# Kernel optimization log

Hardware: AMD Instinct MI355X
Metric: run time of the kernel (lower is better)

Reference implementation:

```python
import jax, jax.numpy as jnp
import numpy as np


def setup_inputs() -> dict:
    key = jax.random.key(0)
    ks = jax.random.split(key, 9)
    B, T, S, E, H = 4, 4096, 4096, 512, 64
    return {
        "x": jax.random.normal(ks[0], (B, T, 1), dtype=jnp.float32),
        "tok_emb": jax.random.normal(ks[1], (B, S, E), dtype=jnp.float32),
        "key_w": jax.random.normal(ks[2], (H, E), dtype=jnp.float32) * 0.05,
        "key_b": jax.random.normal(ks[3], (H,), dtype=jnp.float32) * 0.05,
        "query_w": jax.random.normal(ks[4], (H, 1), dtype=jnp.float32) * 0.05,
        "query_b": jax.random.normal(ks[5], (H,), dtype=jnp.float32) * 0.05,
        "value_w": jax.random.normal(ks[6], (H, E), dtype=jnp.float32) * 0.05,
        "proj_w": jax.random.normal(ks[7], (1, H), dtype=jnp.float32) * 0.05,
        "proj_b": jax.random.normal(ks[8], (1,), dtype=jnp.float32) * 0.05,
    }


def reference(x, tok_emb, key_w, key_b, query_w, query_b, value_w, proj_w, proj_b):
    # k = tanh(Linear(tok_emb))            [B,S,H]
    k = jnp.tanh(jnp.einsum("bse,he->bsh", tok_emb, key_w) + key_b)
    # q = tanh(Linear(x)); x last dim is 1 [B,T,H]
    q = jnp.tanh(jnp.einsum("btu,hu->bth", x, query_w) + query_b)
    scale = k.shape[-1] ** (-0.5)
    wei = jnp.einsum("bth,bsh->bts", q, k) * scale  # [B,T,S]
    # NOTE: softmax over dim=-2 (the query/T axis), faithful to the original
    wei = jax.nn.softmax(wei, axis=-2)
    v = jnp.tanh(jnp.einsum("bse,he->bsh", tok_emb, value_w))  # [B,S,H]
    out = jnp.tanh(jnp.einsum("bts,bsh->bth", wei, v))         # [B,T,H]
    out = jnp.einsum("bth,oh->bto", out, proj_w) + proj_b      # [B,T,1]
    return jnp.squeeze(out, axis=-1)                            # [B,T]
```

## Files before the change

kernel.cpp:

```cpp
#include <hip/hip_runtime.h>
#include <math.h>

#define BB 4
#define TT 4096
#define SS 4096
#define EE 512
#define HH 64
#define NN 128
#define XR 6.0f


typedef __attribute__((ext_vector_type(8))) __bf16 bf16x8;
typedef __attribute__((ext_vector_type(16))) float f32x16;

__device__ __forceinline__ unsigned short f2b(float f) {
  unsigned int u = __float_as_uint(f);
  return (unsigned short)((u + 0x7FFFu + ((u >> 16) & 1u)) >> 16);
}

__device__ __forceinline__ float fast_tanh(float v) {
  float e = __expf(fminf(60.0f, 2.0f * v));
  return (e - 1.0f) * __builtin_amdgcn_rcpf(e + 1.0f);
}

__global__ __launch_bounds__(256) void prep_sm_kernel(
    const float* __restrict__ kw, const float* __restrict__ vw,
    const float* __restrict__ qw, const float* __restrict__ qb,
    const float* __restrict__ x, unsigned int* __restrict__ Wfrag,
    float* __restrict__ Cmat, unsigned short* __restrict__ qnA,
    float* __restrict__ Sm_part, float* __restrict__ Oz) {
  const int blk = blockIdx.x;
  if (blk < 64) {
    int idx = blk * 256 + threadIdx.x;
    int jq = idx & 1;
    int l = (idx >> 1) & 63;
    int ks = (idx >> 7) & 31;
    int nb = idx >> 12;
    int n = nb * 32 + (l & 31);
    int k = ks * 16 + (l >> 5) * 8 + jq * 4;
    const float* row = (n < HH) ? (kw + n * EE + k) : (vw + (n - HH) * EE + k);
    float4 wv = *(const float4*)row;
    Wfrag[idx * 2] = (unsigned int)f2b(wv.x) | ((unsigned int)f2b(wv.y) << 16);
    Wfrag[idx * 2 + 1] =
        (unsigned int)f2b(wv.z) | ((unsigned int)f2b(wv.w) << 16);
  } else if (blk < 128) {
    int idx = (blk - 64) * 256 + threadIdx.x;
    int m = idx >> 7;
    int j = idx & (NN - 1);
    int k = (m * (2 * j + 1)) & 511;
    if (k >= 256) k -= 512;
    Cmat[idx] = cosf((float)k * (float)(M_PI / 256.0));
    if (idx < 8192) ((float4*)Oz)[idx] = make_float4(0.f, 0.f, 0.f, 0.f);
    if (idx < 8192) {
      int h = idx & 63;
      int j2 = idx >> 6;
      float th = (float)M_PI * ((float)j2 + 0.5f) * (1.0f / NN);
      float xj = XR * cosf(th);
      float val = tanhf(fmaf(xj, qw[h], qb[h]));
      int pos =
          (((j2 >> 5) * 4 + (h >> 4)) * 64 + (j2 & 31) + 32 * ((h >> 3) & 1)) *
              8 +
          (h & 7);
      qnA[pos] = f2b(val);
    }
  } else {
    __shared__ float Tm[128][NN + 1];
    int blk2 = blk - 128;
    int b = blk2 >> 5;
    int chunk = blk2 & 31;
    int tid = threadIdx.x;
    if (tid < 128) {
      float xh = x[b * TT + chunk * 128 + tid] * (1.0f / XR);
      xh = fminf(1.0f, fmaxf(-1.0f, xh));
      Tm[tid][0] = 1.0f;
      Tm[tid][1] = xh;
      float x2 = 2.0f * xh;
      float tm2 = 1.0f, tm1 = xh;
#pragma unroll 6
      for (int m = 2; m < NN; ++m) {
        float t = fmaf(x2, tm1, -tm2);
        Tm[tid][m] = t;
        tm2 = tm1;
        tm1 = t;
      }
    }
    __syncthreads();
    if (tid < 128) {
      float s = 0.f;
#pragma unroll 8
      for (int i = 0; i < 128; ++i) s += Tm[i][tid];
      Sm_part[(b * 32 + chunk) * NN + tid] = s;
    }
  }
}

__global__ __launch_bounds__(512) void kvattn_kernel(
    const float* __restrict__ emb, const float* __restrict__ kb,
    const unsigned int* __restrict__ Wfrag, const unsigned short* __restrict__ qnA,
    const float* __restrict__ Cmat, const float* __restrict__ Sm_part,
    float* __restrict__ O) {
  __shared__ __align__(16) char smem[69120];
  unsigned short* A_lds = (unsigned short*)smem;
  unsigned short* ktB = (unsigned short*)smem;
  unsigned short* vB = (unsigned short*)(smem + 8192);
  unsigned short* eA = (unsigned short*)(smem + 16384);
  float* zred = (float*)(smem + 65536);
  float* wql = (float*)(smem + 67840);
  float* izl = (float*)(smem + 68352);
  float* sml = (float*)(smem + 68608);

  const int tid = threadIdx.x;
  const int row0 = blockIdx.x * 64;
  const int bb = row0 >> 12;

  {
    int m = tid >> 3;
    int c8 = tid & 7;
    const float* src = emb + (size_t)(row0 + m) * EE;
    unsigned short* dst = A_lds + (m >> 5) * 16384;
    int ml = m & 31;
    float4 buf[16];
#pragma unroll
    for (int it = 0; it < 16; ++it)
      buf[it] = *(const float4*)(src + (c8 + it * 8) * 4);
#pragma unroll
    for (int it = 0; it < 16; ++it) {
      int k = (c8 + it * 8) * 4;
      float4 v = buf[it];
      int kstep = k >> 4;
      int lane_f = ml + 32 * ((k >> 3) & 1);
      int j = k & 7;
      unsigned int lo = (unsigned int)f2b(v.x) | ((unsigned int)f2b(v.y) << 16);
      unsigned int hi = (unsigned int)f2b(v.z) | ((unsigned int)f2b(v.w) << 16);
      *(uint2*)&dst[(kstep * 64 + lane_f) * 8 + j] = make_uint2(lo, hi);
    }
  }
  if (tid < 128) {
    float s = 0.f;
#pragma unroll 8
    for (int c = 0; c < 32; ++c) s += Sm_part[(bb * 32 + c) * NN + tid];
    sml[tid] = s * ((tid == 0) ? (1.0f / NN) : (2.0f / NN));
  }
  __syncthreads();
  if (tid < 128) {
    float a0 = 0.f, a1 = 0.f, a2 = 0.f, a3 = 0.f;
#pragma unroll
    for (int m = 0; m < NN; m += 4) {
      a0 = fmaf(sml[m], Cmat[m * NN + tid], a0);
      a1 = fmaf(sml[m + 1], Cmat[(m + 1) * NN + tid], a1);
      a2 = fmaf(sml[m + 2], Cmat[(m + 2) * NN + tid], a2);
      a3 = fmaf(sml[m + 3], Cmat[(m + 3) * NN + tid], a3);
    }
    wql[tid] = (a0 + a1) + (a2 + a3);
  }

  const int w8 = tid >> 6;
  const int lane = tid & 63;
  const int w = w8 & 3;
  const int mh = w8 >> 2;
  f32x16 acc = {};
  const bf16x8* Bf = (const bf16x8*)Wfrag;
  const unsigned short* Ah = A_lds + mh * 16384;
#pragma unroll 4
  for (int kstep = 0; kstep < 32; ++kstep) {
    bf16x8 bfr = Bf[(w * 32 + kstep) * 64 + lane];
    bf16x8 a = *(const bf16x8*)&Ah[(kstep * 64 + lane) * 8];
    acc = __builtin_amdgcn_mfma_f32_32x32x16_bf16(a, bfr, acc, 0, 0, 0);
  }
  __syncthreads();

  {
    const int n = w * 32 + (lane & 31);
    if (w < 2) {
      float kbv = kb[n];
      const int ks_h = n >> 4;
      const int off_h = 32 * ((n >> 3) & 1);
      const int jj_h = n & 7;
#pragma unroll
      for (int reg = 0; reg < 16; ++reg) {
        int sl = (reg & 3) + 8 * (reg >> 2) + 4 * (lane >> 5);
        ktB[((mh * 4 + ks_h) * 64 + sl + off_h) * 8 + jj_h] =
            f2b(fast_tanh(acc[reg] + kbv));
      }
    } else {
      int h = n - 64;
      const int nb_h = h >> 5;
      const int lm = h & 31;
#pragma unroll
      for (int reg = 0; reg < 16; ++reg) {
        int sl = (reg & 3) + 8 * (reg >> 2) + 4 * (lane >> 5);
        int s = mh * 32 + sl;
        vB[((nb_h * 4 + (s >> 4)) * 64 + lm + 32 * ((s >> 3) & 1)) * 8 +
           (s & 7)] = f2b(fast_tanh(acc[reg]));
      }
    }
  }
  __syncthreads();

  f32x16 l0 = {};
#pragma unroll
  for (int ks = 0; ks < 4; ++ks) {
    bf16x8 a = *(const bf16x8*)(qnA + ((w * 4 + ks) * 64 + lane) * 8);
    bf16x8 b0 = *(const bf16x8*)&ktB[((mh * 4 + ks) * 64 + lane) * 8];
    l0 = __builtin_amdgcn_mfma_f32_32x32x16_bf16(a, b0, l0, 0, 0, 0);
  }
  float e0[16];
  float zp = 0.f;
#pragma unroll
  for (int r = 0; r < 4; ++r) {
    float4 wq4 = *(const float4*)&wql[w * 32 + 8 * r + 4 * (lane >> 5)];
    float wa[4] = {wq4.x, wq4.y, wq4.z, wq4.w};
#pragma unroll
    for (int c = 0; c < 4; ++c) {
      int reg = 4 * r + c;
      e0[reg] = __expf(l0[reg] * 0.125f);
      zp = fmaf(wa[c], e0[reg], zp);
    }
  }
  zred[(mh * 32 + (lane & 31)) * 9 + w * 2 + (lane >> 5)] = zp;
  __syncthreads();
  if (tid < 64) {
    float sum = 0.f;
#pragma unroll
    for (int k = 0; k < 8; ++k) sum += zred[tid * 9 + k];
    izl[tid] = 1.0f / sum;
  }
  __syncthreads();

  {
    const int s = mh * 32 + (lane & 31);
    const float iz = izl[s];
    const int q0 = w * 4 + (s >> 4);
    const int lof = 32 * ((s >> 3) & 1);
    const int idx = s & 7;
#pragma unroll
    for (int reg = 0; reg < 16; ++reg) {
      int jl = (reg & 3) + 8 * (reg >> 2) + 4 * (lane >> 5);
      eA[(q0 * 64 + jl + lof) * 8 + idx] = f2b(e0[reg] * iz);
    }
  }
  __syncthreads();
  f32x16 o0 = {};
#pragma unroll
  for (int ks = 0; ks < 4; ++ks) {
    bf16x8 a = *(const bf16x8*)&eA[((w * 4 + ks) * 64 + lane) * 8];
    bf16x8 b0 = *(const bf16x8*)&vB[((mh * 4 + ks) * 64 + lane) * 8];
    o0 = __builtin_amdgcn_mfma_f32_32x32x16_bf16(a, b0, o0, 0, 0, 0);
  }
  float* op = O + (size_t)bb * (NN * HH);
  const int h0 = mh * 32 + (lane & 31);
  const int rot = blockIdx.x & 15;
#pragma unroll
  for (int rr = 0; rr < 16; ++rr) {
    int reg = (rr + rot) & 15;
    int j = w * 32 + (reg & 3) + 8 * (reg >> 2) + 4 * (lane >> 5);
    atomicAdd(&op[j * HH + h0], o0[reg]);
  }
}

__global__ __launch_bounds__(256) void final_kernel(
    const float* __restrict__ x, const float* __restrict__ O,
    const float* __restrict__ pw, const float* __restrict__ pb,
    const float* __restrict__ Cmat, float* __restrict__ y) {
  const int idx = blockIdx.x * 256 + threadIdx.x;
  const int b = idx >> 12;
  __shared__ float yl[NN];
  __shared__ float c[NN];
  {
    const int j = threadIdx.x >> 1;
    const int half = threadIdx.x & 1;
    const float4* Ov =
        (const float4*)(O + ((size_t)(b * NN + j) * HH + half * 32));
    const float4* pwv = (const float4*)(pw + half * 32);
    float s = 0.f;
#pragma unroll
    for (int q = 0; q < 8; ++q) {
      float4 ov = Ov[q];
      float4 pv = pwv[q];
      s += fast_tanh(ov.x) * pv.x + fast_tanh(ov.y) * pv.y +
           fast_tanh(ov.z) * pv.z + fast_tanh(ov.w) * pv.w;
    }
    s += __shfl_xor(s, 1, 64);
    if (half == 0) yl[j] = s + pb[0];
  }
  __syncthreads();
  if (threadIdx.x < NN) {
    int m = threadIdx.x;
    double a0 = 0.0, a1 = 0.0;
#pragma unroll 4
    for (int j = 0; j < NN; j += 2) {
      a0 += (double)yl[j] * (double)Cmat[m * NN + j];
      a1 += (double)yl[j + 1] * (double)Cmat[m * NN + j + 1];
    }
    c[m] = (float)((a0 + a1) * ((m == 0 ? 1.0 : 2.0) / NN));
  }
  __syncthreads();
  float xv = x[idx] * (1.0f / XR);
  xv = fminf(1.0f, fmaxf(-1.0f, xv));
  float uu = fmaf(2.0f * xv, xv, -1.0f);
  float tu = 2.0f * uu;
  float be1 = 0.f, be2 = 0.f, bo1 = 0.f, bo2 = 0.f;
  for (int m = 63; m >= 0; --m) {
    float ce = c[2 * m], co = c[2 * m + 1];
    float be = fmaf(tu, be1, ce - be2);
    float bo = fmaf(tu, bo1, co - bo2);
    be2 = be1; be1 = be;
    bo2 = bo1; bo1 = bo;
  }
  float fe = be1 - uu * be2;
  float fo = bo1 - bo2;
  y[idx] = fmaf(xv, fo, fe);
}

extern "C" void kernel_launch(void* const* d_in, const int* in_sizes, int n_in,
                              void* d_out, int out_size, void* d_ws,
                              size_t ws_size, hipStream_t stream) {
  const float* x = (const float*)d_in[0];
  const float* emb = (const float*)d_in[1];
  const float* kw = (const float*)d_in[2];
  const float* kb = (const float*)d_in[3];
  const float* qw = (const float*)d_in[4];
  const float* qb = (const float*)d_in[5];
  const float* vw = (const float*)d_in[6];
  const float* pw = (const float*)d_in[7];
  const float* pb = (const float*)d_in[8];

  float* ws = (float*)d_ws;
  float* O = ws;
  float* Cmat = ws + 32768;
  unsigned short* qnA = (unsigned short*)(Cmat + 16384);
  unsigned int* Wfrag = (unsigned int*)(Cmat + 16384 + 4096);
  float* Sm_part = (float*)(Wfrag + 32768);
  float* y = (float*)d_out;

  prep_sm_kernel<<<256, 256, 0, stream>>>(kw, vw, qw, qb, x, Wfrag, Cmat, qnA,
                                          Sm_part, O);
  kvattn_kernel<<<BB * SS / 64, 512, 0, stream>>>(emb, kb, Wfrag, qnA, Cmat,
                                                  Sm_part, O);
  final_kernel<<<BB * TT / 256, 256, 0, stream>>>(x, O, pw, pb, Cmat, y);
}
```

Baseline: 113.9 us.

## Spread atomic accumulation over eight O slots and reduce in final kernel

Atomic adds into the per-batch output accumulator are spread across eight replicated slots chosen by block index, which reduces contention on the same addresses. The final kernel sums the eight slots before tanh and projection. The embedding load is split into two halves of eight float4 loads, and the kernel gets a launch-bounds occupancy hint of two blocks, both to lower register pressure. In exchange the workspace grows, the prep kernel zeroes the larger O region, and the final kernel does extra reads.

New measurement: 120.6 us. +5.9%, slower.

```diff
diff --git a/kernel.cpp b/kernel.cpp
--- a/kernel.cpp
+++ b/kernel.cpp
@@ -50,7 +50,7 @@
     int k = (m * (2 * j + 1)) & 511;
     if (k >= 256) k -= 512;
     Cmat[idx] = cosf((float)k * (float)(M_PI / 256.0));
-    if (idx < 8192) ((float4*)Oz)[idx] = make_float4(0.f, 0.f, 0.f, 0.f);
+    ((float4*)Oz)[idx] = make_float4(0.f, 0.f, 0.f, 0.f);
     if (idx < 8192) {
       int h = idx & 63;
       int j2 = idx >> 6;
@@ -94,7 +94,7 @@
   }
 }
 
-__global__ __launch_bounds__(512) void kvattn_kernel(
+__global__ __launch_bounds__(512, 2) void kvattn_kernel(
     const float* __restrict__ emb, const float* __restrict__ kb,
     const unsigned int* __restrict__ Wfrag, const unsigned short* __restrict__ qnA,
     const float* __restrict__ Cmat, const float* __restrict__ Sm_part,
@@ -119,20 +119,25 @@
     const float* src = emb + (size_t)(row0 + m) * EE;
     unsigned short* dst = A_lds + (m >> 5) * 16384;
     int ml = m & 31;
-    float4 buf[16];
-#pragma unroll
-    for (int it = 0; it < 16; ++it)
-      buf[it] = *(const float4*)(src + (c8 + it * 8) * 4);
-#pragma unroll
-    for (int it = 0; it < 16; ++it) {
-      int k = (c8 + it * 8) * 4;
-      float4 v = buf[it];
-      int kstep = k >> 4;
-      int lane_f = ml + 32 * ((k >> 3) & 1);
-      int j = k & 7;
-      unsigned int lo = (unsigned int)f2b(v.x) | ((unsigned int)f2b(v.y) << 16);
-      unsigned int hi = (unsigned int)f2b(v.z) | ((unsigned int)f2b(v.w) << 16);
-      *(uint2*)&dst[(kstep * 64 + lane_f) * 8 + j] = make_uint2(lo, hi);
+#pragma unroll
+    for (int half = 0; half < 2; ++half) {
+      float4 buf[8];
+#pragma unroll
+      for (int it = 0; it < 8; ++it)
+        buf[it] = *(const float4*)(src + (c8 + (half * 8 + it) * 8) * 4);
+#pragma unroll
+      for (int it = 0; it < 8; ++it) {
+        int k = (c8 + (half * 8 + it) * 8) * 4;
+        float4 v = buf[it];
+        int kstep = k >> 4;
+        int lane_f = ml + 32 * ((k >> 3) & 1);
+        int j = k & 7;
+        unsigned int lo =
+            (unsigned int)f2b(v.x) | ((unsigned int)f2b(v.y) << 16);
+        unsigned int hi =
+            (unsigned int)f2b(v.z) | ((unsigned int)f2b(v.w) << 16);
+        *(uint2*)&dst[(kstep * 64 + lane_f) * 8 + j] = make_uint2(lo, hi);
+      }
     }
   }
   if (tid < 128) {
@@ -247,7 +252,7 @@
     bf16x8 b0 = *(const bf16x8*)&vB[((mh * 4 + ks) * 64 + lane) * 8];
     o0 = __builtin_amdgcn_mfma_f32_32x32x16_bf16(a, b0, o0, 0, 0, 0);
   }
-  float* op = O + (size_t)bb * (NN * HH);
+  float* op = O + ((size_t)bb * 8 + (blockIdx.x & 7)) * (NN * HH);
   const int h0 = mh * 32 + (lane & 31);
   const int rot = blockIdx.x & 15;
 #pragma unroll
@@ -269,16 +274,27 @@
   {
     const int j = threadIdx.x >> 1;
     const int half = threadIdx.x & 1;
-    const float4* Ov =
-        (const float4*)(O + ((size_t)(b * NN + j) * HH + half * 32));
     const float4* pwv = (const float4*)(pw + half * 32);
+    float4 ov[8];
+#pragma unroll
+    for (int q = 0; q < 8; ++q) ov[q] = make_float4(0.f, 0.f, 0.f, 0.f);
+#pragma unroll
+    for (int slot = 0; slot < 8; ++slot) {
+      const float4* Os =
+          (const float4*)(O + (((size_t)(b * 8 + slot) * NN + j) * HH) +
+                          half * 32);
+#pragma unroll
+      for (int q = 0; q < 8; ++q) {
+        float4 t = Os[q];
+        ov[q].x += t.x; ov[q].y += t.y; ov[q].z += t.z; ov[q].w += t.w;
+      }
+    }
     float s = 0.f;
 #pragma unroll
     for (int q = 0; q < 8; ++q) {
-      float4 ov = Ov[q];
       float4 pv = pwv[q];
-      s += fast_tanh(ov.x) * pv.x + fast_tanh(ov.y) * pv.y +
-           fast_tanh(ov.z) * pv.z + fast_tanh(ov.w) * pv.w;
+      s += fast_tanh(ov[q].x) * pv.x + fast_tanh(ov[q].y) * pv.y +
+           fast_tanh(ov[q].z) * pv.z + fast_tanh(ov[q].w) * pv.w;
     }
     s += __shfl_xor(s, 1, 64);
     if (half == 0) yl[j] = s + pb[0];
@@ -327,7 +343,7 @@
 
   float* ws = (float*)d_ws;
   float* O = ws;
-  float* Cmat = ws + 32768;
+  float* Cmat = ws + 262144;
   unsigned short* qnA = (unsigned short*)(Cmat + 16384);
   unsigned int* Wfrag = (unsigned int*)(Cmat + 16384 + 4096);
   float* Sm_part = (float*)(Wfrag + 32768);
```
